# Kernel tuning notes

Hardware: AMD Instinct MI355X
Metric: run time of the kernel (lower is better)

The kernel has to match this reference:

```python
import jax, jax.numpy as jnp
import numpy as np

N_NODES = 50000
D = 128            # input_dim == hidden_dim == output_dim
N_EDGES = 800000   # 2 relation types concatenated
BN_EPS = 1e-5


def _gcn_conv(x, W, b, src, dst, n):
    # PyG GCNConv: add self loops, symmetric normalization, gather-scatter aggregate.
    h = x @ W                                   # [N, D]
    loop = jnp.arange(n)
    s = jnp.concatenate([src, loop])
    d = jnp.concatenate([dst, loop])
    deg = jax.ops.segment_sum(jnp.ones_like(s, dtype=h.dtype), d, num_segments=n)
    dinv = jnp.where(deg > 0, jax.lax.rsqrt(deg), 0.0)
    norm = dinv[s] * dinv[d]                    # [E+N]
    agg = jax.ops.segment_sum(h[s] * norm[:, None], d, num_segments=n)  # [N, D]
    return agg + b


def _batch_norm(x, gamma, beta):
    # BatchNorm1d training-mode math (biased variance over node axis)
    m = x.mean(axis=0)
    v = x.var(axis=0)
    return (x - m) * jax.lax.rsqrt(v + BN_EPS) * gamma + beta


def _gcn_layer(x, src, dst, W, b, gamma, beta, n):
    h = _gcn_conv(x, W, b, src, dst, n)
    h = jax.nn.relu(_batch_norm(h, gamma, beta))
    return h + x  # residual (in_features == out_features); dropout = identity (eval)


def setup_inputs() -> dict:
    key = jax.random.key(0)
    ks = jax.random.split(key, 8)
    x = jax.random.normal(ks[0], (N_NODES, D), dtype=jnp.float32)
    edge_index = jax.random.randint(ks[1], (2, N_EDGES), 0, N_NODES, dtype=jnp.int64)
    sc = 1.0 / np.sqrt(D)
    return {
        "x": x,
        "edge_index": edge_index,
        "W1": jax.random.normal(ks[2], (D, D), dtype=jnp.float32) * sc,
        "b1": jnp.zeros((D,), dtype=jnp.float32),
        "g1": jnp.ones((D,), dtype=jnp.float32),
        "be1": jnp.zeros((D,), dtype=jnp.float32),
        "W2": jax.random.normal(ks[3], (D, D), dtype=jnp.float32) * sc,
        "b2": jnp.zeros((D,), dtype=jnp.float32),
        "g2": jnp.ones((D,), dtype=jnp.float32),
        "be2": jnp.zeros((D,), dtype=jnp.float32),
        "Wa": jax.random.normal(ks[4], (D, 1), dtype=jnp.float32) * sc,
        "ba": jnp.zeros((1,), dtype=jnp.float32),
    }


def reference(x, edge_index, W1, b1, g1, be1, W2, b2, g2, be2, Wa, ba):
    n = x.shape[0]
    src, dst = edge_index[0], edge_index[1]
    h = _gcn_layer(x, src, dst, W1, b1, g1, be1, n)
    h = _gcn_layer(h, src, dst, W2, b2, g2, be2, n)
    att = jax.nn.softmax(jnp.tanh(h @ Wa + ba), axis=0)  # softmax over nodes
    return h * att
```

## Files before the change

### kernel.cpp

```cpp
#include <hip/hip_runtime.h>
#include <hip/hip_fp16.h>

#define NN 50000
#define DD 128
#define NE 800000
#define BN_EPS 1e-5f
#define NBUCK 196
#define TILE_A 4096
#define SUBCAP 64

typedef _Float16 f16x8 __attribute__((ext_vector_type(8)));
typedef float f32x4 __attribute__((ext_vector_type(4)));

__global__ __launch_bounds__(256) void k_binA(const int* __restrict__ src,
                                              const int* __restrict__ dst,
                                              int* __restrict__ bcnt,
                                              unsigned* __restrict__ evS,
                                              float* __restrict__ sumsZ, int ne) {
    __shared__ int hcnt[NBUCK];
    int tid = threadIdx.x;
    int blk = blockIdx.x;
    if (blk == 0) {
        for (int i = tid; i < 8256; i += 256) sumsZ[i] = 0.f;
    }
    for (int i = tid; i < NBUCK; i += 256) hcnt[i] = 0;
    __syncthreads();
    int base = blk * TILE_A;
    int lim = ne - base;
    if (lim > TILE_A) lim = TILE_A;
    for (int i = tid; i < lim; i += 256) atomicAdd(&hcnt[dst[base + i] >> 8], 1);
    __syncthreads();
    for (int b = tid; b < NBUCK; b += 256) {
        bcnt[b * NBUCK + blk] = hcnt[b];
        hcnt[b] = 0;
    }
    __syncthreads();
    for (int i = tid; i < lim; i += 256) {
        int d = dst[base + i];
        int s = src[base + i];
        int bk = d >> 8;
        int rank = atomicAdd(&hcnt[bk], 1);
        if (rank < SUBCAP)
            evS[(size_t)(bk * NBUCK + blk) * SUBCAP + rank] =
                (unsigned)s | ((unsigned)(d & 255) << 16);
    }
}

__global__ __launch_bounds__(256) void k_binB(const unsigned* __restrict__ evS,
                                              const int* __restrict__ bcnt,
                                              unsigned* __restrict__ ev,
                                              int* __restrict__ rowp,
                                              float* __restrict__ dinv, int n) {
    __shared__ int sc[256];
    __shared__ int ncnt[256];
    __shared__ int ncur[256];
    __shared__ int s_lo, s_cnt;
    int tid = threadIdx.x;
    int b = blockIdx.x;

    int tot = 0;
    if (tid < NBUCK) {
        const int* row = bcnt + tid * NBUCK;
        for (int j = 0; j < NBUCK; j++) {
            int c = row[j];
            tot += (c > SUBCAP) ? SUBCAP : c;
        }
    }
    sc[tid] = tot;
    __syncthreads();
    for (int off = 1; off < 256; off <<= 1) {
        int add = (tid >= off) ? sc[tid - off] : 0;
        __syncthreads();
        sc[tid] += add;
        __syncthreads();
    }
    if (tid == b) { s_lo = sc[tid] - tot; s_cnt = tot; }
    __syncthreads();
    int lo = s_lo;
    int cnt_b = s_cnt;

    int c = 0;
    if (tid < NBUCK) {
        c = bcnt[b * NBUCK + tid];
        if (c > SUBCAP) c = SUBCAP;
    }
    size_t sbase = (size_t)(b * NBUCK + tid) * SUBCAP;

    ncnt[tid] = 0;
    __syncthreads();
    for (int r = 0; r < c; r++)
        atomicAdd(&ncnt[evS[sbase + r] >> 16], 1);
    __syncthreads();
    int nv = ncnt[tid];
    sc[tid] = nv;
    __syncthreads();
    for (int off = 1; off < 256; off <<= 1) {
        int add = (tid >= off) ? sc[tid - off] : 0;
        __syncthreads();
        sc[tid] += add;
        __syncthreads();
    }
    int nb = sc[tid] - nv;
    ncur[tid] = nb;
    int node = (b << 8) + tid;
    if (node < n) {
        rowp[node] = lo + nb;
        dinv[node] = 1.0f / sqrtf((float)(nv + 1));
    }
    if (b == NBUCK - 1 && tid == 0) rowp[n] = lo + cnt_b;
    __syncthreads();
    for (int r = 0; r < c; r++) {
        unsigned rec = evS[sbase + r];
        int ln = rec >> 16;
        int pos = atomicAdd(&ncur[ln], 1);
        ev[lo + pos] = rec & 0xFFFFu;
    }
}

#define GTILE 64
#define GEMM_GRID 512
__global__ __launch_bounds__(256) void k_gemm(const float* __restrict__ A,
                                              const __half* __restrict__ A16,
                                              const float* __restrict__ res,
                                              const float* __restrict__ sums,
                                              const float* __restrict__ gamma,
                                              const float* __restrict__ beta,
                                              __half* __restrict__ Hout,
                                              const float* __restrict__ dscale,
                                              const float* __restrict__ W,
                                              __half* __restrict__ C, int n) {
    __shared__ __half sW[DD * DD];
    __shared__ __half sA[GTILE * DD];
    __shared__ float s_scale[DD], s_shift[DD];
    int tid = threadIdx.x;
    int wave = tid >> 6;
    int lane = tid & 63;
    bool fused = (res != nullptr);

    {
        for (int s = tid; s < DD * DD / 8; s += 256) {
            int l = s & 63;
            int ks = (s >> 6) & 3;
            int cb = s >> 8;
            int col = cb * 16 + (l & 15);
            int kbase = ks * 32 + (l >> 4) * 8;
            __align__(16) __half tmp[8];
            #pragma unroll
            for (int j = 0; j < 8; j++)
                tmp[j] = __float2half_rn(W[(kbase + j) * DD + col]);
            *(uint4*)(sW + s * 8) = *(uint4*)tmp;
        }
    }
    if (fused && tid < DD) {
        float ssum = 0.f, qsum = 0.f;
        #pragma unroll
        for (int b = 0; b < 16; b++) {
            ssum += sums[b * 256 + tid];
            qsum += sums[b * 256 + 128 + tid];
        }
        float inv_n = 1.0f / (float)n;
        float mean = ssum * inv_n;
        float var = qsum * inv_n - mean * mean;
        float sc = gamma[tid] * (1.0f / sqrtf(var + BN_EPS));
        s_scale[tid] = sc;
        s_shift[tid] = beta[tid] - mean * sc;
    }

    int ntiles = (n + GTILE - 1) / GTILE;
    for (int t = blockIdx.x; t < ntiles; t += gridDim.x) {
        int row0 = t * GTILE;
        __syncthreads();
        {
            for (int i = tid; i < GTILE * DD / 4; i += 256) {
                int r = i >> 5;
                int kq = i & 31;
                bool rowok = (row0 + r < n);
                float4 v = make_float4(0.f, 0.f, 0.f, 0.f);
                if (rowok) {
                    if (A16 != nullptr) {
                        uint2 rawv = ((const uint2*)(A16 + (size_t)row0 * DD))[i];
                        const __half2* ap = (const __half2*)&rawv;
                        float2 a0 = __half22float2(ap[0]);
                        float2 a1 = __half22float2(ap[1]);
                        v = make_float4(a0.x, a0.y, a1.x, a1.y);
                    } else {
                        v = ((const float4*)(A + (size_t)row0 * DD))[i];
                    }
                }
                if (fused) {
                    float4 rv = make_float4(0.f, 0.f, 0.f, 0.f);
                    if (rowok) rv = ((const float4*)(res + (size_t)row0 * DD))[i];
                    int f4 = kq * 4;
                    v.x = fmaxf(v.x * s_scale[f4]     + s_shift[f4],     0.f) + rv.x;
                    v.y = fmaxf(v.y * s_scale[f4 + 1] + s_shift[f4 + 1], 0.f) + rv.y;
                    v.z = fmaxf(v.z * s_scale[f4 + 2] + s_shift[f4 + 2], 0.f) + rv.z;
                    v.w = fmaxf(v.w * s_scale[f4 + 3] + s_shift[f4 + 3], 0.f) + rv.w;
                }
                __half2 p0 = __floats2half2_rn(v.x, v.y);
                __half2 p1 = __floats2half2_rn(v.z, v.w);
                uint2 pk;
                pk.x = *(unsigned*)&p0;
                pk.y = *(unsigned*)&p1;
                if (fused && rowok)
                    ((uint2*)(Hout + (size_t)row0 * DD))[i] = pk;
                int slot = ((r >> 4) * 4 + (kq >> 3)) * 64 +
                           (((kq >> 1) & 3) << 4) + (r & 15);
                int byte = slot * 16 + (kq & 1) * 8;
                byte ^= ((byte >> 9) & 7) << 4;
                *(uint2*)((char*)sA + byte) = pk;
            }
        }
        __syncthreads();

        f32x4 acc[8];
        #pragma unroll
        for (int cb = 0; cb < 8; cb++) acc[cb] = (f32x4)(0.0f);
        f16x8 af[4];
        #pragma unroll
        for (int ks = 0; ks < 4; ks++) {
            int rb = ((wave * 4 + ks) * 64 + lane) * 16;
            rb ^= ((rb >> 9) & 7) << 4;
            af[ks] = *(const f16x8*)((const char*)sA + rb);
        }
        #pragma unroll
        for (int cb = 0; cb < 8; cb++) {
            #pragma unroll
            for (int ks = 0; ks < 4; ks++) {
                f16x8 bf = *(const f16x8*)(sW + ((cb * 4 + ks) * 64 + lane) * 8);
                acc[cb] = __builtin_amdgcn_mfma_f32_16x16x32_f16(af[ks], bf,
                                                                 acc[cb], 0, 0, 0);
            }
        }

        __syncthreads();

        float dv[4];
        #pragma unroll
        for (int rr = 0; rr < 4; rr++) {
            int row = row0 + wave * 16 + (lane >> 4) * 4 + rr;
            dv[rr] = (row < n) ? dscale[row] : 1.f;
        }

        __half* sC = sA + wave * (16 * DD);
        #pragma unroll
        for (int cb = 0; cb < 8; cb++) {
            int col = cb * 16 + (lane & 15);
            #pragma unroll
            for (int rr = 0; rr < 4; rr++) {
                int grow = (lane >> 4) * 4 + rr;
                sC[grow * DD + (col ^ ((grow & 3) << 4))] =
                    __float2half(acc[cb][rr] * dv[rr]);
            }
        }
        __syncthreads();
        #pragma unroll
        for (int i2 = 0; i2 < 4; i2++) {
            int o = (i2 * 64 + lane) * 8;
            int grow = o >> 7;
            int col0 = o & 127;
            int row = row0 + wave * 16 + grow;
            if (row < n) {
                uint4 val = *(uint4*)(sC + grow * DD + (col0 ^ ((grow & 3) << 4)));
                *(uint4*)(C + (size_t)row * DD + col0) = val;
            }
        }
    }
}

#define ACC8T(acc, raw) { const __half2* hp_ = (const __half2*)&(raw);         \
    float2 c0_ = __half22float2(hp_[0]); float2 c1_ = __half22float2(hp_[1]);  \
    float2 c2_ = __half22float2(hp_[2]); float2 c3_ = __half22float2(hp_[3]);  \
    acc[0] += c0_.x; acc[1] += c0_.y; acc[2] += c1_.x; acc[3] += c1_.y;        \
    acc[4] += c2_.x; acc[5] += c2_.y; acc[6] += c3_.x; acc[7] += c3_.y; }

__global__ __launch_bounds__(256) void k_agg(const __half* __restrict__ h,
                                             const int* __restrict__ rowp,
                                             const unsigned* __restrict__ ev,
                                             const float* __restrict__ dinv,
                                             const float* __restrict__ bias,
                                             __half* __restrict__ out,
                                             float* __restrict__ sums, int n) {
    int tid = threadIdx.x;
    int grp = tid >> 4;
    int m = tid & 15;
    int node = blockIdx.x * 16 + grp;
    bool activ = node < n;

    int beg = 0, end = 0;
    float di = 0.f;
    if (activ) { beg = rowp[node]; end = rowp[node + 1]; di = dinv[node]; }

    float sf[8] = {0.f, 0.f, 0.f, 0.f, 0.f, 0.f, 0.f, 0.f};
    float bf[8];
    {
        float4 b0 = *(const float4*)(bias + m * 8);
        float4 b1 = *(const float4*)(bias + m * 8 + 4);
        bf[0] = b0.x; bf[1] = b0.y; bf[2] = b0.z; bf[3] = b0.w;
        bf[4] = b1.x; bf[5] = b1.y; bf[6] = b1.z; bf[7] = b1.w;
        if (activ) {
            float4 raw = *(const float4*)(h + (size_t)node * DD + m * 8);
            const __half2* hp = (const __half2*)&raw;
            float2 s0 = __half22float2(hp[0]);
            float2 s1 = __half22float2(hp[1]);
            float2 s2 = __half22float2(hp[2]);
            float2 s3 = __half22float2(hp[3]);
            sf[0] = s0.x; sf[1] = s0.y; sf[2] = s1.x; sf[3] = s1.y;
            sf[4] = s2.x; sf[5] = s2.y; sf[6] = s3.x; sf[7] = s3.y;
        }
    }

    float a[8] = {0.f, 0.f, 0.f, 0.f, 0.f, 0.f, 0.f, 0.f};
    float a2[8] = {0.f, 0.f, 0.f, 0.f, 0.f, 0.f, 0.f, 0.f};
    int e = beg;
    int cnt4 = (end - beg) >> 2;
    if (cnt4 > 0) {
        unsigned s0 = ev[e], s1 = ev[e + 1], s2 = ev[e + 2], s3 = ev[e + 3];
        float4 r0 = *(const float4*)(h + (size_t)s0 * DD + m * 8);
        float4 r1 = *(const float4*)(h + (size_t)s1 * DD + m * 8);
        float4 r2 = *(const float4*)(h + (size_t)s2 * DD + m * 8);
        float4 r3 = *(const float4*)(h + (size_t)s3 * DD + m * 8);
        for (int g = 1; g < cnt4; g++) {
            e += 4;
            unsigned t0 = ev[e], t1 = ev[e + 1], t2 = ev[e + 2], t3 = ev[e + 3];
            float4 q0 = *(const float4*)(h + (size_t)t0 * DD + m * 8);
            float4 q1 = *(const float4*)(h + (size_t)t1 * DD + m * 8);
            float4 q2 = *(const float4*)(h + (size_t)t2 * DD + m * 8);
            float4 q3 = *(const float4*)(h + (size_t)t3 * DD + m * 8);
            ACC8T(a, r0); ACC8T(a2, r1); ACC8T(a, r2); ACC8T(a2, r3);
            r0 = q0; r1 = q1; r2 = q2; r3 = q3;
        }
        ACC8T(a, r0); ACC8T(a2, r1); ACC8T(a, r2); ACC8T(a2, r3);
        e += 4;
    }
    for (; e < end; e++) {
        unsigned s = ev[e];
        float4 raw = *(const float4*)(h + (size_t)s * DD + m * 8);
        ACC8T(a, raw);
    }
    #pragma unroll
    for (int j = 0; j < 8; j++) a[j] += a2[j];

    float o[8];
    #pragma unroll
    for (int j = 0; j < 8; j++) o[j] = di * (a[j] + sf[j]) + bf[j];
    if (activ) {
        __half2 p0 = __floats2half2_rn(o[0], o[1]);
        __half2 p1 = __floats2half2_rn(o[2], o[3]);
        __half2 p2 = __floats2half2_rn(o[4], o[5]);
        __half2 p3 = __floats2half2_rn(o[6], o[7]);
        uint4 pk;
        pk.x = *(unsigned*)&p0; pk.y = *(unsigned*)&p1;
        pk.z = *(unsigned*)&p2; pk.w = *(unsigned*)&p3;
        *(uint4*)(out + (size_t)node * DD + m * 8) = pk;
    }

    __shared__ float rs[16][132];
    #pragma unroll
    for (int j = 0; j < 8; j++) rs[grp][m * 8 + j] = activ ? o[j] : 0.f;
    __syncthreads();

    int bank = blockIdx.x & 15;
    if (tid < 128) {
        float s = 0.f;
        #pragma unroll
        for (int r2 = 0; r2 < 16; r2++) s += rs[r2][tid];
        atomicAdd(&sums[bank * 256 + tid], s);
    } else {
        int f = tid - 128;
        float q = 0.f;
        #pragma unroll
        for (int r2 = 0; r2 < 16; r2++) { float v = rs[r2][f]; q += v * v; }
        atomicAdd(&sums[bank * 256 + 128 + f], q);
    }
}

__global__ __launch_bounds__(256) void k_bn(const __half* __restrict__ X,
                                            const __half* __restrict__ res,
                                            const float* __restrict__ sums,
                                            const float* __restrict__ gamma,
                                            const float* __restrict__ beta,
                                            const float* __restrict__ Wa,
                                            const float* __restrict__ ba,
                                            __half* __restrict__ out,
                                            float* __restrict__ evec,
                                            float* __restrict__ Zb, int n) {
    __shared__ float s_scale[128], s_shift[128];
    if (threadIdx.x < 128) {
        int ff = threadIdx.x;
        float ssum = 0.f, qsum = 0.f;
        #pragma unroll
        for (int b = 0; b < 16; b++) {
            ssum += sums[b * 256 + ff];
            qsum += sums[b * 256 + 128 + ff];
        }
        float inv_n = 1.0f / (float)n;
        float mean = ssum * inv_n;
        float var = qsum * inv_n - mean * mean;
        float sc = gamma[ff] * (1.0f / sqrtf(var + BN_EPS));
        s_scale[ff] = sc;
        s_shift[ff] = beta[ff] - mean * sc;
    }
    __syncthreads();
    int idx = blockIdx.x * 256 + threadIdx.x;
    int total = n * (DD / 4);
    int f = (threadIdx.x & 31) * 4;
    float o[4] = {0.f, 0.f, 0.f, 0.f};
    if (idx < total) {
        uint2 xv = ((const uint2*)X)[idx];
        uint2 rw = ((const uint2*)res)[idx];
        const __half2* xp = (const __half2*)&xv;
        const __half2* rp = (const __half2*)&rw;
        float2 x0 = __half22float2(xp[0]), x1 = __half22float2(xp[1]);
        float2 r0 = __half22float2(rp[0]), r1 = __half22float2(rp[1]);
        float vi[4] = {x0.x, x0.y, x1.x, x1.y};
        float ri[4] = {r0.x, r0.y, r1.x, r1.y};
        #pragma unroll
        for (int j = 0; j < 4; j++) {
            float x = vi[j] * s_scale[f + j] + s_shift[f + j];
            x = fmaxf(x, 0.f);
            o[j] = x + ri[j];
        }
        __half2 o0 = __floats2half2_rn(o[0], o[1]);
        __half2 o1 = __floats2half2_rn(o[2], o[3]);
        uint2 ov;
        ov.x = *(unsigned*)&o0;
        ov.y = *(unsigned*)&o1;
        ((uint2*)out)[idx] = ov;
    }
    if (Wa != nullptr) {
        float t = 0.f;
        if (idx < total) {
            float4 wv = *(const float4*)(Wa + f);
            t = o[0] * wv.x + o[1] * wv.y + o[2] * wv.z + o[3] * wv.w;
        }
        #pragma unroll
        for (int m = 16; m >= 1; m >>= 1) t += __shfl_xor(t, m);
        __shared__ float part[8];
        if ((threadIdx.x & 31) == 0) {
            float ev = 0.f;
            if (idx < total) {
                ev = expf(tanhf(t + ba[0]));
                evec[idx >> 5] = ev;
            }
            part[threadIdx.x >> 5] = ev;
        }
        __syncthreads();
        if (threadIdx.x == 0) {
            float z = part[0] + part[1] + part[2] + part[3] +
                      part[4] + part[5] + part[6] + part[7];
            atomicAdd(&Zb[blockIdx.x & 63], z);
        }
    }
}

__global__ __launch_bounds__(256) void k_out(const __half* __restrict__ H,
                                             const float* __restrict__ evec,
                                             const float* __restrict__ Zb,
                                             float* __restrict__ out, int n) {
    __shared__ float sZ;
    if (threadIdx.x == 0) {
        float z = 0.f;
        #pragma unroll
        for (int i = 0; i < 64; i++) z += Zb[i];
        sZ = z;
    }
    __syncthreads();
    int idx = blockIdx.x * blockDim.x + threadIdx.x;
    int total = n * (DD / 4);
    if (idx >= total) return;
    int node = idx >> 5;
    float s = evec[node] / sZ;
    uint2 hv = ((const uint2*)H)[idx];
    const __half2* hp = (const __half2*)&hv;
    float2 h0 = __half22float2(hp[0]), h1 = __half22float2(hp[1]);
    ((float4*)out)[idx] = make_float4(h0.x * s, h0.y * s, h1.x * s, h1.y * s);
}

extern "C" void kernel_launch(void* const* d_in, const int* in_sizes, int n_in,
                              void* d_out, int out_size, void* d_ws, size_t ws_size,
                              hipStream_t stream) {
    const float* x   = (const float*)d_in[0];
    const int* eidx  = (const int*)d_in[1];
    const float* W1  = (const float*)d_in[2];
    const float* b1  = (const float*)d_in[3];
    const float* g1  = (const float*)d_in[4];
    const float* be1 = (const float*)d_in[5];
    const float* W2  = (const float*)d_in[6];
    const float* b2  = (const float*)d_in[7];
    const float* g2  = (const float*)d_in[8];
    const float* be2 = (const float*)d_in[9];
    const float* Wa  = (const float*)d_in[10];
    const float* ba  = (const float*)d_in[11];
    float* out = (float*)d_out;

    const int* srcp = eidx;
    const int* dstp = eidx + NE;

    float* bufA = (float*)d_ws;
    float* bufB = bufA + (size_t)NN * DD;
    float* bufC = bufB + (size_t)NN * DD;
    unsigned* ev = (unsigned*)(bufC + (size_t)NN * DD);
    float* dinv = (float*)(ev + NE);
    float* evec = dinv + NN;
    int* bcnt   = (int*)(evec + NN);
    float* sums = (float*)(bcnt + 38656);
    float* Zb   = sums + 8192;
    int* rowp   = (int*)(Zb + 64);

    __half* hH  = (__half*)bufA;
    unsigned* evS = (unsigned*)bufB;
    __half* hAgg = (__half*)bufB;
    __half* hRes = (__half*)bufC;

    float* sumsL1 = sums;
    float* sumsL2 = sums + 4096;

    const int nA = (NE + TILE_A - 1) / TILE_A;
    k_binA<<<nA, 256, 0, stream>>>(srcp, dstp, bcnt, evS, sums, NE);
    k_binB<<<NBUCK, 256, 0, stream>>>(evS, bcnt, ev, rowp, dinv, NN);

    int agg_grid  = (NN + 15) / 16;
    int ew_grid   = (NN * (DD / 4) + 255) / 256;

    k_gemm<<<GEMM_GRID, 256, 0, stream>>>(x, nullptr, nullptr, nullptr, nullptr,
                                          nullptr, nullptr, dinv, W1, hH, NN);
    k_agg<<<agg_grid, 256, 0, stream>>>(hH, rowp, ev, dinv, b1, hAgg, sumsL1, NN);

    k_gemm<<<GEMM_GRID, 256, 0, stream>>>(nullptr, hAgg, x, sumsL1, g1, be1,
                                          hRes, dinv, W2, hH, NN);
    k_agg<<<agg_grid, 256, 0, stream>>>(hH, rowp, ev, dinv, b2, hAgg, sumsL2, NN);
    k_bn<<<ew_grid, 256, 0, stream>>>(hAgg, hRes, sumsL2, g2, be2, Wa, ba,
                                      hRes, evec, Zb, NN);

    k_out<<<ew_grid, 256, 0, stream>>>(hRes, evec, Zb, out, NN);
}
```

Measured before the change: 257.0 us.

## Split aggregation feature dimension across two grid columns with 8 lanes per node

The gather-aggregate kernel now splits the 128 features into two 64-channel halves via blockIdx.y, using 8 lanes per node and 32 nodes per block instead of 16 lanes and 16 nodes. Each gathered row segment becomes 128 bytes instead of 256, so more nodes are in flight per block and each half's working set of h is smaller, which may help L2 locality. In exchange, the edge list and row pointers are read twice, and each 64-byte lane group does less work per edge index load.

```diff
diff --git a/kernel.cpp b/kernel.cpp
--- a/kernel.cpp
+++ b/kernel.cpp
@@ -281,10 +281,14 @@
                                              __half* __restrict__ out,
                                              float* __restrict__ sums, int n) {
     int tid = threadIdx.x;
-    int grp = tid >> 4;
-    int m = tid & 15;
-    int node = blockIdx.x * 16 + grp;
+    int grp = tid >> 3;
+    int m = tid & 7;
+    int y = blockIdx.y;
+    int choff = y * 64;
+    int node = blockIdx.x * 32 + grp;
     bool activ = node < n;
+
+    const __half* hh = h + choff;
 
     int beg = 0, end = 0;
     float di = 0.f;
@@ -293,12 +297,12 @@
     float sf[8] = {0.f, 0.f, 0.f, 0.f, 0.f, 0.f, 0.f, 0.f};
     float bf[8];
     {
-        float4 b0 = *(const float4*)(bias + m * 8);
-        float4 b1 = *(const float4*)(bias + m * 8 + 4);
+        float4 b0 = *(const float4*)(bias + choff + m * 8);
+        float4 b1 = *(const float4*)(bias + choff + m * 8 + 4);
         bf[0] = b0.x; bf[1] = b0.y; bf[2] = b0.z; bf[3] = b0.w;
         bf[4] = b1.x; bf[5] = b1.y; bf[6] = b1.z; bf[7] = b1.w;
         if (activ) {
-            float4 raw = *(const float4*)(h + (size_t)node * DD + m * 8);
+            float4 raw = *(const float4*)(hh + (size_t)node * DD + m * 8);
             const __half2* hp = (const __half2*)&raw;
             float2 s0 = __half22float2(hp[0]);
             float2 s1 = __half22float2(hp[1]);
@@ -315,17 +319,17 @@
     int cnt4 = (end - beg) >> 2;
     if (cnt4 > 0) {
         unsigned s0 = ev[e], s1 = ev[e + 1], s2 = ev[e + 2], s3 = ev[e + 3];
-        float4 r0 = *(const float4*)(h + (size_t)s0 * DD + m * 8);
-        float4 r1 = *(const float4*)(h + (size_t)s1 * DD + m * 8);
-        float4 r2 = *(const float4*)(h + (size_t)s2 * DD + m * 8);
-        float4 r3 = *(const float4*)(h + (size_t)s3 * DD + m * 8);
+        float4 r0 = *(const float4*)(hh + (size_t)s0 * DD + m * 8);
+        float4 r1 = *(const float4*)(hh + (size_t)s1 * DD + m * 8);
+        float4 r2 = *(const float4*)(hh + (size_t)s2 * DD + m * 8);
+        float4 r3 = *(const float4*)(hh + (size_t)s3 * DD + m * 8);
         for (int g = 1; g < cnt4; g++) {
             e += 4;
             unsigned t0 = ev[e], t1 = ev[e + 1], t2 = ev[e + 2], t3 = ev[e + 3];
-            float4 q0 = *(const float4*)(h + (size_t)t0 * DD + m * 8);
-            float4 q1 = *(const float4*)(h + (size_t)t1 * DD + m * 8);
-            float4 q2 = *(const float4*)(h + (size_t)t2 * DD + m * 8);
-            float4 q3 = *(const float4*)(h + (size_t)t3 * DD + m * 8);
+            float4 q0 = *(const float4*)(hh + (size_t)t0 * DD + m * 8);
+            float4 q1 = *(const float4*)(hh + (size_t)t1 * DD + m * 8);
+            float4 q2 = *(const float4*)(hh + (size_t)t2 * DD + m * 8);
+            float4 q3 = *(const float4*)(hh + (size_t)t3 * DD + m * 8);
             ACC8T(a, r0); ACC8T(a2, r1); ACC8T(a, r2); ACC8T(a2, r3);
             r0 = q0; r1 = q1; r2 = q2; r3 = q3;
         }
@@ -334,7 +338,7 @@
     }
     for (; e < end; e++) {
         unsigned s = ev[e];
-        float4 raw = *(const float4*)(h + (size_t)s * DD + m * 8);
+        float4 raw = *(const float4*)(hh + (size_t)s * DD + m * 8);
         ACC8T(a, raw);
     }
     #pragma unroll
@@ -351,26 +355,26 @@
         uint4 pk;
         pk.x = *(unsigned*)&p0; pk.y = *(unsigned*)&p1;
         pk.z = *(unsigned*)&p2; pk.w = *(unsigned*)&p3;
-        *(uint4*)(out + (size_t)node * DD + m * 8) = pk;
-    }
-
-    __shared__ float rs[16][132];
+        *(uint4*)(out + (size_t)node * DD + choff + m * 8) = pk;
+    }
+
+    __shared__ float rs[32][66];
     #pragma unroll
     for (int j = 0; j < 8; j++) rs[grp][m * 8 + j] = activ ? o[j] : 0.f;
     __syncthreads();
 
     int bank = blockIdx.x & 15;
-    if (tid < 128) {
+    if (tid < 64) {
         float s = 0.f;
         #pragma unroll
-        for (int r2 = 0; r2 < 16; r2++) s += rs[r2][tid];
-        atomicAdd(&sums[bank * 256 + tid], s);
-    } else {
-        int f = tid - 128;
+        for (int r2 = 0; r2 < 32; r2++) s += rs[r2][tid];
+        atomicAdd(&sums[bank * 256 + choff + tid], s);
+    } else if (tid < 128) {
+        int f = tid - 64;
         float q = 0.f;
         #pragma unroll
-        for (int r2 = 0; r2 < 16; r2++) { float v = rs[r2][f]; q += v * v; }
-        atomicAdd(&sums[bank * 256 + 128 + f], q);
+        for (int r2 = 0; r2 < 32; r2++) { float v = rs[r2][f]; q += v * v; }
+        atomicAdd(&sums[bank * 256 + 128 + choff + f], q);
     }
 }
 
@@ -519,7 +523,7 @@
     k_binA<<<nA, 256, 0, stream>>>(srcp, dstp, bcnt, evS, sums, NE);
     k_binB<<<NBUCK, 256, 0, stream>>>(evS, bcnt, ev, rowp, dinv, NN);
 
-    int agg_grid  = (NN + 15) / 16;
+    dim3 agg_grid((NN + 31) / 32, 2);
     int ew_grid   = (NN * (DD / 4) + 255) / 256;
 
     k_gemm<<<GEMM_GRID, 256, 0, stream>>>(x, nullptr, nullptr, nullptr, nullptr,
```

Result: no change. 257.7 us (+0.3%).
